# Kernel optimization log

Hardware: AMD Instinct MI355X
Metric: run time of the kernel (lower is better)

The kernel has to match this reference:

```python
import jax, jax.numpy as jnp
import numpy as np

EPS = 1e-5


def _resize_bilinear_ac(x, h, w):
    # bilinear, align_corners=True; x: [B, C, H, W]
    H, W = x.shape[2], x.shape[3]
    ys = jnp.linspace(0.0, H - 1.0, h)
    xs = jnp.linspace(0.0, W - 1.0, w)
    y0 = jnp.floor(ys).astype(jnp.int32)
    x0 = jnp.floor(xs).astype(jnp.int32)
    y1 = jnp.clip(y0 + 1, 0, H - 1)
    x1 = jnp.clip(x0 + 1, 0, W - 1)
    wy = (ys - y0.astype(ys.dtype))[None, None, :, None]
    wx = (xs - x0.astype(xs.dtype))[None, None, None, :]
    rows0 = x[:, :, y0, :]  # [B,C,h,W]
    rows1 = x[:, :, y1, :]
    a = rows0[:, :, :, x0]
    b = rows0[:, :, :, x1]
    c = rows1[:, :, :, x0]
    d = rows1[:, :, :, x1]
    top = a * (1.0 - wx) + b * wx
    bot = c * (1.0 - wx) + d * wx
    return top * (1.0 - wy) + bot * wy


def _conv3x3(x, w):
    return jax.lax.conv_general_dilated(
        x, w, window_strides=(1, 1), padding=[(1, 1), (1, 1)],
        dimension_numbers=('NCHW', 'OIHW', 'NCHW'))


def _bn(x, g, b, m, v):
    scale = (g / jnp.sqrt(v + EPS))[None, :, None, None]
    shift = (b - m * g / jnp.sqrt(v + EPS))[None, :, None, None]
    return x * scale + shift


def setup_inputs() -> dict:
    key = jax.random.key(0)
    ks = jax.random.split(key, 12)
    B = 8
    xt = jax.random.normal(ks[0], (B, 512, 32, 32), jnp.float32)
    xm = jax.random.normal(ks[1], (B, 512, 64, 64), jnp.float32)
    xl = jax.random.normal(ks[2], (B, 256, 128, 128), jnp.float32)
    alpha = jnp.ones((1,), jnp.float32)
    w0 = jax.random.normal(ks[3], (512, 512, 3, 3), jnp.float32) * 0.02
    g0 = jnp.abs(jax.random.normal(ks[4], (512,), jnp.float32)) * 0.1 + 1.0
    b0 = jax.random.normal(ks[5], (512,), jnp.float32) * 0.1
    m0 = jax.random.normal(ks[6], (512,), jnp.float32) * 0.1
    v0 = jnp.abs(jax.random.normal(ks[7], (512,), jnp.float32)) * 0.1 + 1.0
    w1 = jax.random.normal(ks[8], (256, 512, 3, 3), jnp.float32) * 0.02
    g1 = jnp.abs(jax.random.normal(ks[9], (256,), jnp.float32)) * 0.1 + 1.0
    b1 = jax.random.normal(ks[10], (256,), jnp.float32) * 0.1
    m1 = jax.random.normal(ks[11], (256,), jnp.float32) * 0.1
    v1 = jnp.abs(jax.random.normal(jax.random.fold_in(key, 99), (256,), jnp.float32)) * 0.1 + 1.0
    return {"xt": xt, "xm": xm, "xl": xl, "alpha": alpha,
            "w0": w0, "g0": g0, "b0": b0, "m0": m0, "v0": v0,
            "w1": w1, "g1": g1, "b1": b1, "m1": m1, "v1": v1}


def reference(xt, xm, xl, alpha, w0, g0, b0, m0, v0, w1, g1, b1, m1, v1):
    # DecoderModule.forward: upsample xt to xm size (align_corners=True),
    # fuse with alpha-weighted skip, conv0(512->512,BN,ReLU), conv1(512->256,BN,ReLU).
    # xl is accepted but unused in this forward (as in the source).
    h, w = xm.shape[2], xm.shape[3]
    xup = _resize_bilinear_ac(xt, h, w)
    xfuse = xup + alpha[0] * xm
    x = jax.nn.relu(_bn(_conv3x3(xfuse, w0), g0, b0, m0, v0))
    xt_fea = jax.nn.relu(_bn(_conv3x3(x, w1), g1, b1, m1, v1))
    return xt_fea
```

## Files before the change

kernel.cpp:

```cpp
#include <hip/hip_runtime.h>
#include <stdint.h>

#define EPSV 1e-5f

#define CPLANE 278784

using floatx4 = __attribute__((ext_vector_type(4))) float;
using short8  = __attribute__((ext_vector_type(8))) short;

#define GLD(gp, lp) __builtin_amdgcn_global_load_lds( \
    (const __attribute__((address_space(1))) void*)(gp), \
    (__attribute__((address_space(3))) void*)(lp), 16, 0, 0)

__device__ __forceinline__ unsigned short f2bf(float f) {
  union { float f; unsigned int u; } x; x.f = f;
  unsigned int r = x.u + 0x7fffu + ((x.u >> 16) & 1u);
  return (unsigned short)(r >> 16);
}

__global__ __launch_bounds__(256) void border_zero_kernel(
    unsigned short* __restrict__ Xp0, unsigned short* __restrict__ Xp1) {
  int idx = blockIdx.x * 256 + threadIdx.x;
  int k = idx % 260;
  int rest = idx / 260;
  int cc = rest & 63;
  int b = rest >> 6;
  int py, px;
  if (k < 66)       { py = 0;  px = k; }
  else if (k < 132) { py = 65; px = k - 66; }
  else { int k2 = k - 132; py = 1 + (k2 >> 1); px = (k2 & 1) ? 65 : 0; }
  int off = cc * CPLANE + ((b * 66 + py) * 66 + px) * 8;
  short8 z = {};
  *(short8*)(Xp0 + off) = z;
  *(short8*)(Xp1 + off) = z;
}

__global__ __launch_bounds__(256) void fuse_upsample_kernel(
    const float* __restrict__ xt, const float* __restrict__ xm,
    const float* __restrict__ alpha, unsigned short* __restrict__ Xp) {
  __shared__ float sm[32 * 66];
  __shared__ float st[2 * 32 * 34];

  const int tid = threadIdx.x;
  const int ct = blockIdx.x & 15;
  const int y  = (blockIdx.x >> 4) & 63;
  const int b  = blockIdx.x >> 10;
  const int c0 = ct * 32;

  const float fy = y * (31.0f / 63.0f);
  const int y0 = (int)fy;
  const float wy = fy - (float)y0;
  const int y1 = min(y0 + 1, 31);

  {
    const int cb = (tid >> 6) * 8;
    const int xi = tid & 63;
#pragma unroll
    for (int j = 0; j < 8; ++j) {
      int c = cb + j;
      sm[c * 66 + xi] = xm[(((b << 9) + c0 + c) << 12) + (y << 6) + xi];
    }
  }
#pragma unroll
  for (int j = 0; j < 8; ++j) {
    int idx = j * 256 + tid;
    int xi = idx & 31, cc = (idx >> 5) & 31, h = idx >> 10;
    int yr = h ? y1 : y0;
    st[h * 1088 + cc * 34 + xi] =
        xt[(((b << 9) + c0 + cc) << 10) + (yr << 5) + xi];
  }
  __syncthreads();

  const float a = alpha[0];
  const int xo = tid & 63;
  const int cl = tid >> 6;
  const float fx = xo * (31.0f / 63.0f);
  const int x0 = (int)fx;
  const float wx = fx - (float)x0;
  const int x1 = min(x0 + 1, 31);
  short8 ov;
#pragma unroll
  for (int j = 0; j < 8; ++j) {
    int c = cl * 8 + j;
    float t0 = st[c * 34 + x0], t1 = st[c * 34 + x1];
    float u0 = st[1088 + c * 34 + x0], u1 = st[1088 + c * 34 + x1];
    float top = t0 * (1.0f - wx) + t1 * wx;
    float bot = u0 * (1.0f - wx) + u1 * wx;
    float up = top * (1.0f - wy) + bot * wy;
    float val = up + a * sm[c * 66 + xo];
    ov[j] = (short)f2bf(val);
  }
  *(short8*)(Xp + ((c0 >> 3) + cl) * CPLANE +
             ((b * 66 + y + 1) * 66 + xo + 1) * 8) = ov;
}

template <int COUT>
__global__ __launch_bounds__(256) void prep_w_kernel(
    const float* __restrict__ w, unsigned short* __restrict__ Wg) {
  __shared__ unsigned short l[4608];
  const int o = blockIdx.x, t = threadIdx.x;
  const float* src = w + o * 4608;
#pragma unroll
  for (int j = 0; j < 18; ++j) {
    int idx = j * 256 + t;
    l[(idx % 9) * 512 + idx / 9] = f2bf(src[idx]);
  }
  __syncthreads();
#pragma unroll
  for (int tap = 0; tap < 9; ++tap) {
    int cc = t >> 2;
    int off = ((tap * 64 + cc) * COUT + o) * 8 + ((2 * t) & 7);
    *(unsigned int*)(Wg + off) = *(const unsigned int*)(l + (tap << 9) + 2 * t);
  }
}

template <int COUT, bool FINAL>
__global__ __launch_bounds__(512, 2) void conv3x3_fat_kernel(
    const unsigned short* __restrict__ Xp, const unsigned short* __restrict__ Wg,
    const float* __restrict__ gamma, const float* __restrict__ beta,
    const float* __restrict__ mean, const float* __restrict__ var,
    unsigned short* __restrict__ OutPad, float* __restrict__ OutF) {
  constexpr int NCT = COUT / 256;
  constexpr int NWG = 128 * NCT;
  constexpr int QXC = NWG / 8;
  constexpr int AKS = 3176;
  constexpr int BKS = 2056;
  __shared__ unsigned short Abuf[8 * AKS];
  __shared__ unsigned short Bbuf0[8 * BKS];
  __shared__ unsigned short Bbuf1[8 * BKS];

  const int tid = threadIdx.x;
  const int w = tid >> 6;
  const int lane = tid & 63;
  const int wm = w >> 2;
  const int wn = w & 3;
  const int fi = lane & 15;
  const int kc4 = lane >> 4;

  const int bid = (int)blockIdx.x;
  const int logical = (bid & 7) * QXC + (bid >> 3);
  const int ptile = logical & 127;
  const int ctile = logical >> 7;
  const int p0 = ptile * 256;
  const int pb = p0 >> 12;
  const int y0 = (p0 >> 6) & 63;
  const int arowg = ((pb * 66 + y0) * 66) * 8;

  floatx4 acc[8][4] = {};

  auto stageA = [&](int cg) {
    const unsigned short* g = Xp + (cg * 8 + w) * CPLANE + arowg + lane * 8;
    unsigned short* d = Abuf + w * AKS;
#pragma unroll
    for (int rr = 0; rr < 6; ++rr) {
      GLD(g + rr * 528,      d + rr * 528);
      GLD(g + rr * 528 + 16, d + rr * 528 + 16);
    }
  };
  auto stageB = [&](int tap, int cg, unsigned short* dst) {
    const unsigned short* g =
        Wg + ((tap * 64 + cg * 8 + w) * COUT + ctile * 256) * 8 + lane * 8;
    unsigned short* d = dst + w * BKS;
#pragma unroll
    for (int ch = 0; ch < 4; ++ch) GLD(g + ch * 512, d + ch * 512);
  };
  auto compute = [&](const unsigned short* Bsel, int dy, int dx) {
#pragma unroll
    for (int t = 0; t < 2; ++t) {
      const unsigned short* ab = Abuf + (kc4 + 4 * t) * AKS;
      short8 af[8];
#pragma unroll
      for (int mi = 0; mi < 8; ++mi)
        af[mi] = *(const short8*)(ab + (wm * 2 + (mi >> 2) + 1 + dy) * 528 +
                                  ((mi & 3) * 16 + fi + 1 + dx) * 8);
      const unsigned short* bb =
          Bsel + (kc4 + 4 * t) * BKS + (wn * 64 + fi) * 8;
      short8 bfr[4];
#pragma unroll
      for (int ni = 0; ni < 4; ++ni)
        bfr[ni] = *(const short8*)(bb + ni * 128);
#pragma unroll
      for (int mi = 0; mi < 8; ++mi)
#pragma unroll
        for (int ni = 0; ni < 4; ++ni)
          acc[mi][ni] = __builtin_amdgcn_mfma_f32_16x16x32_bf16(
              af[mi], bfr[ni], acc[mi][ni], 0, 0, 0);
    }
  };

  int buf = 0;
  stageA(0);
  stageB(0, 0, Bbuf0);
  __syncthreads();
  for (int cg = 0; cg < 8; ++cg) {
#pragma unroll
    for (int tap = 0; tap < 9; ++tap) {
      unsigned short* cur = buf ? Bbuf1 : Bbuf0;
      unsigned short* nxt = buf ? Bbuf0 : Bbuf1;
      if (tap < 8)      stageB(tap + 1, cg, nxt);
      else if (cg < 7)  stageB(0, cg + 1, nxt);
      compute(cur, tap / 3 - 1, tap % 3 - 1);
      __syncthreads();
      buf ^= 1;
    }
    if (cg < 7) {
      stageA(cg + 1);
      __syncthreads();
    }
  }

#pragma unroll
  for (int ni = 0; ni < 4; ++ni) {
    const int co = ctile * 256 + wn * 64 + ni * 16 + fi;
    const float sc = gamma[co] / sqrtf(var[co] + EPSV);
    const float sh2 = beta[co] - mean[co] * sc;
#pragma unroll
    for (int mi = 0; mi < 8; ++mi) {
      const int p = p0 + wm * 128 + mi * 16 + kc4 * 4;
      const int pbb = p >> 12;
      const int prem = p & 4095;
      if constexpr (FINAL) {
        floatx4 o;
#pragma unroll
        for (int r = 0; r < 4; ++r) o[r] = fmaxf(acc[mi][ni][r] * sc + sh2, 0.0f);
        *(floatx4*)(OutF + ((pbb * COUT + co) << 12) + prem) = o;
      } else {
        const int py = prem >> 6, px = prem & 63;
        unsigned short* dst = OutPad + (co >> 3) * CPLANE +
            ((pbb * 66 + py + 1) * 66 + px + 1) * 8 + (co & 7);
#pragma unroll
        for (int r = 0; r < 4; ++r)
          dst[r * 8] = f2bf(fmaxf(acc[mi][ni][r] * sc + sh2, 0.0f));
      }
    }
  }
}

template <int COUT, int CTILE, bool FINAL>
__global__ __launch_bounds__(256) void conv3x3_kernel(
    const unsigned short* __restrict__ Xp, const unsigned short* __restrict__ Wg,
    const float* __restrict__ gamma, const float* __restrict__ beta,
    const float* __restrict__ mean, const float* __restrict__ var,
    unsigned short* __restrict__ OutPad, float* __restrict__ OutF) {
  constexpr int NCT = COUT / CTILE;
  constexpr int NI  = CTILE / 32;
  constexpr int NWG = 256 * NCT;
  constexpr int QXC = NWG / 8;
  __shared__ unsigned short Abuf[16896];
  __shared__ unsigned short Bbuf0[CTILE * 64];
  __shared__ unsigned short Bbuf1[CTILE * 64];

  const int tid = threadIdx.x;
  const int bid = (int)blockIdx.x;
  const int logical = (bid & 7) * QXC + (bid >> 3);
  const int ptile = logical & 255;
  const int ctile = logical >> 8;
  const int p0 = ptile * 128;
  const int w = tid >> 6;
  const int lane = tid & 63;

  const int pb = p0 >> 12;
  const int yb = (p0 >> 6) & 63;
  const int arowg = ((pb * 66 + yb) * 66) * 8;

  const int fi = lane & 15;
  const int kc = lane >> 4;
  const int wm = w >> 1, wn = w & 1;
  const int aLane = kc * 2112 + (wm + 1) * 528 + (fi + 1) * 8;
  const int bLane = kc * CTILE * 8 + (wn * (CTILE / 2) + fi) * 8;

  floatx4 acc[4][NI] = {};

  auto stageA = [&](int cg) {
#pragma unroll
    for (int kk = 0; kk < 2; ++kk) {
      const int kc2 = 2 * w + kk;
      const unsigned short* g = Xp + (cg * 8 + kc2) * CPLANE + arowg + lane * 8;
      unsigned short* d = Abuf + kc2 * 2112;
#pragma unroll
      for (int rr = 0; rr < 4; ++rr) {
        GLD(g + rr * 528,      d + rr * 528);
        GLD(g + rr * 528 + 16, d + rr * 528 + 16);
      }
    }
  };
  auto stageB = [&](int tap, int cg, unsigned short* dst) {
#pragma unroll
    for (int kk = 0; kk < 2; ++kk) {
      const int kc2 = 2 * w + kk;
      const unsigned short* g =
          Wg + ((tap * 64 + cg * 8 + kc2) * COUT + ctile * CTILE + lane) * 8;
#pragma unroll
      for (int half = 0; half < CTILE / 64; ++half)
        GLD(g + half * 64 * 8, dst + (kc2 * CTILE + half * 64) * 8);
    }
  };
  auto compute = [&](const unsigned short* Bsel, int dy, int dx) {
#pragma unroll
    for (int t = 0; t < 2; ++t) {
      short8 af[4];
#pragma unroll
      for (int mi = 0; mi < 4; ++mi)
        af[mi] = *(const short8*)(Abuf + aLane + t * 8448 + dy * 528 +
                                  (mi * 16 + dx) * 8);
      short8 bfr[NI];
#pragma unroll
      for (int ni = 0; ni < NI; ++ni)
        bfr[ni] = *(const short8*)(Bsel + bLane + t * CTILE * 32 + ni * 128);
#pragma unroll
      for (int mi = 0; mi < 4; ++mi)
#pragma unroll
        for (int ni = 0; ni < NI; ++ni)
          acc[mi][ni] = __builtin_amdgcn_mfma_f32_16x16x32_bf16(
              af[mi], bfr[ni], acc[mi][ni], 0, 0, 0);
    }
  };

  int buf = 0;
  stageA(0);
  stageB(0, 0, Bbuf0);
  __syncthreads();
  for (int cg = 0; cg < 8; ++cg) {
#pragma unroll
    for (int tap = 0; tap < 9; ++tap) {
      unsigned short* cur = buf ? Bbuf1 : Bbuf0;
      unsigned short* nxt = buf ? Bbuf0 : Bbuf1;
      if (tap < 8)      stageB(tap + 1, cg, nxt);
      else if (cg < 7)  stageB(0, cg + 1, nxt);
      compute(cur, tap / 3 - 1, tap % 3 - 1);
      __syncthreads();
      buf ^= 1;
    }
    if (cg < 7) {
      stageA(cg + 1);
      __syncthreads();
    }
  }

#pragma unroll
  for (int ni = 0; ni < NI; ++ni) {
    const int co = ctile * CTILE + wn * (CTILE / 2) + ni * 16 + fi;
    const float sc = gamma[co] / sqrtf(var[co] + EPSV);
    const float sh2 = beta[co] - mean[co] * sc;
#pragma unroll
    for (int mi = 0; mi < 4; ++mi) {
      const int p = p0 + wm * 64 + mi * 16 + kc * 4;
      const int pbb = p >> 12;
      const int prem = p & 4095;
      if constexpr (FINAL) {
        floatx4 o;
#pragma unroll
        for (int r = 0; r < 4; ++r) o[r] = fmaxf(acc[mi][ni][r] * sc + sh2, 0.0f);
        *(floatx4*)(OutF + ((pbb * COUT + co) << 12) + prem) = o;
      } else {
        const int py = prem >> 6, px = prem & 63;
        unsigned short* dst = OutPad + (co >> 3) * CPLANE +
            ((pbb * 66 + py + 1) * 66 + px + 1) * 8 + (co & 7);
#pragma unroll
        for (int r = 0; r < 4; ++r)
          dst[r * 8] = f2bf(fmaxf(acc[mi][ni][r] * sc + sh2, 0.0f));
      }
    }
  }
}

extern "C" void kernel_launch(void* const* d_in, const int* in_sizes, int n_in,
                              void* d_out, int out_size, void* d_ws, size_t ws_size,
                              hipStream_t stream) {
  const float* xt    = (const float*)d_in[0];
  const float* xm    = (const float*)d_in[1];
  const float* alpha = (const float*)d_in[3];
  const float* w0    = (const float*)d_in[4];
  const float* g0    = (const float*)d_in[5];
  const float* b0    = (const float*)d_in[6];
  const float* m0    = (const float*)d_in[7];
  const float* v0    = (const float*)d_in[8];
  const float* w1    = (const float*)d_in[9];
  const float* g1    = (const float*)d_in[10];
  const float* b1    = (const float*)d_in[11];
  const float* m1    = (const float*)d_in[12];
  const float* v1    = (const float*)d_in[13];
  float* out = (float*)d_out;

  char* ws = (char*)d_ws;
  unsigned short* Xp0 = (unsigned short*)(ws);
  unsigned short* Xp1 = (unsigned short*)(ws + 35684352);
  unsigned short* Wg0 = (unsigned short*)(ws + 2 * 35684352);
  unsigned short* Wg1 = (unsigned short*)(ws + 2 * 35684352 + 4718592);

  border_zero_kernel<<<520, 256, 0, stream>>>(Xp0, Xp1);
  prep_w_kernel<512><<<512, 256, 0, stream>>>(w0, Wg0);
  prep_w_kernel<256><<<256, 256, 0, stream>>>(w1, Wg1);
  fuse_upsample_kernel<<<8192, 256, 0, stream>>>(xt, xm, alpha, Xp0);
  conv3x3_fat_kernel<512, false><<<256, 512, 0, stream>>>(Xp0, Wg0, g0, b0, m0, v0, Xp1, nullptr);
  conv3x3_kernel<256, 128, true><<<512, 256, 0, stream>>>(Xp1, Wg1, g1, b1, m1, v1, nullptr, out);
}
```

Before: 450.9 us.

## Triple-buffer weight tiles with prefetch distance two and partial vmcnt waits

Replaces the double-buffered B (weight) staging in the fat conv kernel with three LDS buffers, so weights are prefetched two taps ahead. The full __syncthreads is replaced by an explicit s_waitcnt vmcnt(4) plus s_barrier, so the most recent prefetch can stay in flight across the barrier. The last channel group is peeled into its own loop. This is meant to hide global-to-LDS latency behind the MFMA work. In exchange it uses more LDS, and correctness depends on the vmcnt count matching the number of loads each stageB issues.

```diff
diff --git a/kernel.cpp b/kernel.cpp
--- a/kernel.cpp
+++ b/kernel.cpp
@@ -122,12 +122,11 @@
     unsigned short* __restrict__ OutPad, float* __restrict__ OutF) {
   constexpr int NCT = COUT / 256;
   constexpr int NWG = 128 * NCT;
-  constexpr int QXC = NWG / 8;
+  constexpr int QPX = NWG / 8;
   constexpr int AKS = 3176;
   constexpr int BKS = 2056;
   __shared__ unsigned short Abuf[8 * AKS];
-  __shared__ unsigned short Bbuf0[8 * BKS];
-  __shared__ unsigned short Bbuf1[8 * BKS];
+  __shared__ unsigned short Bbuf[3][8 * BKS];
 
   const int tid = threadIdx.x;
   const int w = tid >> 6;
@@ -138,7 +137,7 @@
   const int kc4 = lane >> 4;
 
   const int bid = (int)blockIdx.x;
-  const int logical = (bid & 7) * QXC + (bid >> 3);
+  const int logical = (bid & 7) * QPX + (bid >> 3);
   const int ptile = logical & 127;
   const int ctile = logical >> 7;
   const int p0 = ptile * 256;
@@ -188,25 +187,32 @@
     }
   };
 
-  int buf = 0;
   stageA(0);
-  stageB(0, 0, Bbuf0);
-  __syncthreads();
-  for (int cg = 0; cg < 8; ++cg) {
+  stageB(0, 0, Bbuf[0]);
+  stageB(1, 0, Bbuf[1]);
+  asm volatile("s_waitcnt vmcnt(0)" ::: "memory");
+  __builtin_amdgcn_s_barrier();
+
+  for (int cg = 0; cg < 7; ++cg) {
 #pragma unroll
     for (int tap = 0; tap < 9; ++tap) {
-      unsigned short* cur = buf ? Bbuf1 : Bbuf0;
-      unsigned short* nxt = buf ? Bbuf0 : Bbuf1;
-      if (tap < 8)      stageB(tap + 1, cg, nxt);
-      else if (cg < 7)  stageB(0, cg + 1, nxt);
-      compute(cur, tap / 3 - 1, tap % 3 - 1);
-      __syncthreads();
-      buf ^= 1;
-    }
-    if (cg < 7) {
-      stageA(cg + 1);
-      __syncthreads();
-    }
+      if (tap < 7) stageB(tap + 2, cg,     Bbuf[(tap + 2) % 3]);
+      else         stageB(tap - 7, cg + 1, Bbuf[(tap + 2) % 3]);
+      compute(Bbuf[tap % 3], tap / 3 - 1, tap % 3 - 1);
+      asm volatile("s_waitcnt vmcnt(4)" ::: "memory");
+      __builtin_amdgcn_s_barrier();
+      if (tap == 8) {
+        stageA(cg + 1);
+        asm volatile("s_waitcnt vmcnt(0)" ::: "memory");
+        __builtin_amdgcn_s_barrier();
+      }
+    }
+  }
+#pragma unroll
+  for (int tap = 0; tap < 9; ++tap) {
+    if (tap < 7) stageB(tap + 2, 7, Bbuf[(tap + 2) % 3]);
+    compute(Bbuf[tap % 3], tap / 3 - 1, tap % 3 - 1);
+    __syncthreads();
   }
 
 #pragma unroll
@@ -245,14 +251,14 @@
   constexpr int NCT = COUT / CTILE;
   constexpr int NI  = CTILE / 32;
   constexpr int NWG = 256 * NCT;
-  constexpr int QXC = NWG / 8;
+  constexpr int QPX = NWG / 8;
   __shared__ unsigned short Abuf[16896];
   __shared__ unsigned short Bbuf0[CTILE * 64];
   __shared__ unsigned short Bbuf1[CTILE * 64];
 
   const int tid = threadIdx.x;
   const int bid = (int)blockIdx.x;
-  const int logical = (bid & 7) * QXC + (bid >> 3);
+  const int logical = (bid & 7) * QPX + (bid >> 3);
   const int ptile = logical & 255;
   const int ctile = logical >> 8;
   const int p0 = ptile * 128;
```

Result: no change. 459.6 us (+1.9%).
